# Optimization experiments

Hardware: AMD Instinct MI355X
Metric: run time of the kernel (lower is better)

Reference implementation:

```python
import jax, jax.numpy as jnp
import numpy as np

B = 256       # batch
IN_N = 64     # in_n_capsules
CS = 16       # input_size == current spatial size (child k=1,s=1,p=0)
HID = 128     # linformer hidden_dim
OUT_N = 32    # out_n_capsules
D = 16        # in_d_capsules == out_d_capsules (pose dim)
MPD = 4       # matrix_pose_dim = sqrt(D)
EPS = 1e-5
SCALE = D ** (-0.5)  # pose_dim ** -0.5 used in routing dots


def setup_inputs() -> dict:
    key = jax.random.key(0)
    ks = jax.random.split(key, 6)
    current_pose = jax.random.normal(ks[0], (B, IN_N, CS, CS, D), jnp.float32)
    next_pose = jax.random.normal(ks[1], (B, OUT_N, D), jnp.float32)
    w_current = 0.02 * jax.random.normal(ks[2], (IN_N, MPD, MPD), jnp.float32)
    w_next = 0.02 * jax.random.normal(ks[3], (OUT_N, MPD, MPD), jnp.float32)
    E_proj = 0.02 * jax.random.normal(ks[4], (IN_N, CS * CS, HID), jnp.float32)
    ln_weight = jnp.ones((D,), jnp.float32)
    ln_bias = jnp.zeros((D,), jnp.float32)
    return {
        'current_pose': current_pose, 'next_pose': next_pose,
        'w_current': w_current, 'w_next': w_next, 'E_proj': E_proj,
        'ln_weight': ln_weight, 'ln_bias': ln_bias, 'num_iter': 1,
    }


def reference(current_pose, next_pose, w_current, w_next, E_proj, ln_weight, ln_bias, num_iter):
    # ---- child matrix-pose bilinear transform ----
    # [B*CS*CS, IN_N, 4, 4] @ [1, IN_N, 4, 4]
    cp = current_pose.reshape(B * CS * CS, IN_N, MPD, MPD)
    cp = jnp.matmul(cp, w_current[None])
    # ---- Linformer headwise projection over spatial positions ----
    cp = cp.reshape(B, D, IN_N, 1, CS * CS)
    k_val = jnp.matmul(cp, E_proj[None]).squeeze(3)        # [B, D, IN_N, HID]
    k_val = k_val.reshape(B, D, IN_N * HID).transpose(0, 2, 1)  # [B, new_n, D]
    # ---- parent matrix-pose transform of next_pose (query) ----
    q = next_pose.reshape(B, OUT_N, MPD, MPD)
    q = jnp.matmul(w_next[None], q).reshape(B, OUT_N, D)   # [B, OUT_N, D]
    # ---- dot-product routing: softmax over parent capsules (dim -2) ----
    dots = jax.nn.softmax(jnp.einsum('bje,bie->bji', q, k_val) * SCALE, axis=-2)
    cand = jnp.einsum('bji,bie->bje', dots, k_val)          # [B, OUT_N, D]
    # ---- parent matrix-pose transform of candidates ----
    cand = jnp.matmul(w_next[None], cand.reshape(B, OUT_N, MPD, MPD))
    cand = cand.reshape(B, 1, 1, OUT_N, D)[:, 0]            # squeeze(1) -> [B, 1, OUT_N, D]
    # ---- dropout(p=0) is identity; LayerNorm over last dim ----
    mu = jnp.mean(cand, axis=-1, keepdims=True)
    var = jnp.mean((cand - mu) ** 2, axis=-1, keepdims=True)
    return (cand - mu) / jnp.sqrt(var + EPS) * ln_weight + ln_bias
```

## Files before the change

kernel.cpp:

```cpp
#include <hip/hip_runtime.h>
#include <cstdint>

#define EPSF 1e-5f
#define SCALEF 0.25f

typedef __attribute__((ext_vector_type(8))) __fp16 f16x8;
typedef __attribute__((ext_vector_type(2))) __fp16 f16x2;
typedef __attribute__((ext_vector_type(4))) float f32x4;

union U4H8 { uint4 u; f16x8 v; unsigned short s[8]; };
union U1H2 { unsigned u; f16x2 h; };

__device__ __forceinline__ uint32_t pk2h(float a, float b){
    union { f16x2 h; uint32_t u; } c;
    c.h = __builtin_amdgcn_cvt_pkrtz(a, b);
    return c.u;
}
__device__ __forceinline__ void gload_lds16(const void* g, void* l){
    __builtin_amdgcn_global_load_lds((const __attribute__((address_space(1))) uint32_t*)g,
                                     (__attribute__((address_space(3))) uint32_t*)l, 16, 0, 0);
}


__global__ void k_init(const float* __restrict__ wc, const float* __restrict__ E,
                       const float* __restrict__ npse, const float* __restrict__ wnx,
                       unsigned short* __restrict__ Ft, float* __restrict__ q2g){
    const int blk = blockIdx.x;
    const int tid = threadIdx.x;
    if (blk < 1024){
        const int n2 = blk >> 4, x = blk & 15;
        const int h = tid;
        const int j = (n2 & 3) * 16 + x;
        float w[16];
#pragma unroll
        for (int t = 0; t < 16; ++t) w[t] = wc[j * 16 + t];
        const float* Eb = E + ((size_t)n2 * 256 + x * 16) * 128 + h;
        float e[16];
#pragma unroll
        for (int t = 0; t < 16; ++t) e[t] = Eb[(size_t)t * 128];
        float v[16];
#pragma unroll
        for (int dd = 0; dd < 16; ++dd){
            const int r = dd >> 2, k = dd & 3;
            float acc = 0.f;
#pragma unroll
            for (int c = 0; c < 4; ++c) acc += w[k * 4 + c] * e[r * 4 + c];
            v[dd] = acc;
        }
        uint32_t pk[8];
#pragma unroll
        for (int q = 0; q < 8; ++q) pk[q] = pk2h(v[q * 2], v[q * 2 + 1]);
        unsigned short* dst = Ft + (size_t)n2 * 32768 + (size_t)h * 256 + x * 16;
        ((uint4*)dst)[0] = make_uint4(pk[0], pk[1], pk[2], pk[3]);
        ((uint4*)dst)[1] = make_uint4(pk[4], pk[5], pk[6], pk[7]);
    } else {
        const int b = blk - 1024;
#pragma unroll
        for (int q = 0; q < 4; ++q){
            const int t = q * 128 + tid;
            const int o = t >> 4, d = t & 15, r = d >> 2, c = d & 3;
            float acc = 0.f;
#pragma unroll
            for (int k = 0; k < 4; ++k)
                acc += wnx[o * 16 + r * 4 + k] * npse[((size_t)b * 32 + o) * 16 + k * 4 + c];
            q2g[(size_t)b * 512 + t] = acc * SCALEF;
        }
    }
}

__global__ __launch_bounds__(256, 4) void k_gemm(const float* __restrict__ cp,
                                                 const unsigned short* __restrict__ Ft,
                                                 const float* __restrict__ q2g,
                                                 unsigned short* __restrict__ Pmid){
    __shared__ __align__(16) char smem[40960];
    unsigned short (*As)[4096] = (unsigned short (*)[4096])smem;
    unsigned short (*Fs)[4096] = (unsigned short (*)[4096])(smem + 16384);
    const int tid  = threadIdx.x;
    const int lane = tid & 63;
    const int wave = tid >> 6;
    const int wm = wave >> 1, wn2 = wave & 1;
    const int l15 = lane & 15, g = lane >> 4;
    const int mtile = blockIdx.x;
    const int n2 = blockIdx.y;
    const int n2h = n2 >> 4, y = n2 & 15;

    const float* abase[4];
    int aoff[4];
#pragma unroll
    for (int p = 0; p < 4; ++p){
        const int idx = tid + p * 256;
        const int m = idx >> 3;
        const int kq = idx & 7;
        const int b = mtile * 8 + (m >> 4);
        const int i = (m & 15) * 4 + n2h;
        abase[p] = cp + (size_t)b * 262144 + (size_t)i * 4096 + (size_t)y * 256 + kq * 4;
        aoff[p] = m * 32 + (((kq >> 1) ^ ((m >> 1) & 3)) * 8) + (kq & 1) * 4;
    }
    const unsigned short* bsrc[2];
    unsigned short* bdst[2];
#pragma unroll
    for (int p = 0; p < 2; ++p){
        const int idx = tid + p * 256;
        const int h = idx >> 2;
        const int kq4 = idx & 3;
        bsrc[p] = Ft + (size_t)n2 * 32768 + (size_t)h * 256 + ((kq4 ^ ((h >> 1) & 3)) * 8);
        bdst[p] = &Fs[0][(size_t)(p * 256 + (tid & ~63)) * 8];
    }
    int afoff[4], bfoff[4];
#pragma unroll
    for (int mf = 0; mf < 4; ++mf){
        const int row = wm * 64 + mf * 16 + l15;
        afoff[mf] = row * 32 + ((g ^ ((row >> 1) & 3)) * 8);
    }
#pragma unroll
    for (int nf = 0; nf < 4; ++nf){
        const int row = wn2 * 64 + nf * 16 + l15;
        bfoff[nf] = row * 32 + ((g ^ ((row >> 1) & 3)) * 8);
    }

    f32x4 acc[4][4];
#pragma unroll
    for (int mf = 0; mf < 4; ++mf)
#pragma unroll
        for (int nf = 0; nf < 4; ++nf) acc[mf][nf] = (f32x4){0.f, 0.f, 0.f, 0.f};

    float4 av[4];
#pragma unroll
    for (int p = 0; p < 2; ++p) gload_lds16(bsrc[p], bdst[p]);
#pragma unroll
    for (int p = 0; p < 2; ++p) gload_lds16(bsrc[p] + 32, bdst[p] + 4096);
#pragma unroll
    for (int p = 0; p < 4; ++p) av[p] = *(const float4*)(abase[p]);
#pragma unroll
    for (int p = 0; p < 4; ++p){
        uint2 w2 = make_uint2(pk2h(av[p].x, av[p].y), pk2h(av[p].z, av[p].w));
        *(uint2*)(&As[0][aoff[p]]) = w2;
    }
    __syncthreads();

#pragma unroll
    for (int kt = 0; kt < 8; ++kt){
        if (kt < 7){
#pragma unroll
            for (int p = 0; p < 4; ++p) av[p] = *(const float4*)(abase[p] + (kt + 1) * 32);
        }
        __builtin_amdgcn_sched_barrier(0);
        if (kt < 6){
#pragma unroll
            for (int p = 0; p < 2; ++p)
                gload_lds16(bsrc[p] + (kt + 2) * 32, bdst[p] + ((kt + 2) % 3) * 4096);
        }
        f16x8 af[4], bfr[4];
#pragma unroll
        for (int mf = 0; mf < 4; ++mf) af[mf] = *(const f16x8*)(&As[kt & 1][afoff[mf]]);
#pragma unroll
        for (int nf = 0; nf < 4; ++nf) bfr[nf] = *(const f16x8*)(&Fs[kt % 3][bfoff[nf]]);
#pragma unroll
        for (int nf = 0; nf < 4; ++nf)
#pragma unroll
            for (int mf = 0; mf < 4; ++mf)
                acc[mf][nf] = __builtin_amdgcn_mfma_f32_16x16x32_f16(af[mf], bfr[nf], acc[mf][nf], 0, 0, 0);
        if (kt < 7){
#pragma unroll
            for (int p = 0; p < 4; ++p){
                uint2 w2 = make_uint2(pk2h(av[p].x, av[p].y), pk2h(av[p].z, av[p].w));
                *(uint2*)(&As[(kt + 1) & 1][aoff[p]]) = w2;
            }
        }
        if (kt < 6){ asm volatile("s_waitcnt vmcnt(2) lgkmcnt(0)" ::: "memory"); }
        else       { asm volatile("s_waitcnt vmcnt(0) lgkmcnt(0)" ::: "memory"); }
        __builtin_amdgcn_s_barrier();
        __builtin_amdgcn_sched_barrier(0);
    }

    char* eb  = smem + wave * 6144;
    char* kvT = eb;
    char* wJ  = eb + 2048;
    const f32x4 zf = (f32x4){0.f, 0.f, 0.f, 0.f};
    f32x4 pvm[4][2];

#pragma unroll
    for (int mf = 0; mf < 4; ++mf){
        const int b = mtile * 8 + wm * 4 + mf;
        U4H8 aq[2];
#pragma unroll
        for (int jh = 0; jh < 2; ++jh){
            const float4 q = *(const float4*)(q2g + (size_t)b * 512
                                              + (size_t)(jh * 16 + l15) * 16 + g * 4);
            aq[jh].u = make_uint4(pk2h(q.x, q.y), pk2h(q.z, q.w), 0u, 0u);
        }
        f32x4 pv0 = zf, pv1 = zf;
#pragma unroll
        for (int nf = 0; nf < 4; ++nf){
            U4H8 B;
            B.u = make_uint4(pk2h(acc[mf][nf][0], acc[mf][nf][1]),
                             pk2h(acc[mf][nf][2], acc[mf][nf][3]), 0u, 0u);
            const int ncol2 = (nf * 16 + l15) * 2;
#pragma unroll
            for (int r = 0; r < 4; ++r){
                const int e = g * 4 + r;
                *(unsigned short*)(kvT + e * 128 + (ncol2 ^ ((e & 7) << 4))) = B.s[r];
            }
            f32x4 s0 = __builtin_amdgcn_mfma_f32_16x16x32_f16(aq[0].v, B.v, zf, 0, 0, 0);
            f32x4 s1 = __builtin_amdgcn_mfma_f32_16x16x32_f16(aq[1].v, B.v, zf, 0, 0, 0);
            float e0[4], e1[4];
#pragma unroll
            for (int r = 0; r < 4; ++r){ e0[r] = __expf(s0[r]); e1[r] = __expf(s1[r]); }
            float ts = ((e0[0] + e0[1]) + (e0[2] + e0[3]))
                     + ((e1[0] + e1[1]) + (e1[2] + e1[3]));
            ts += __shfl_xor(ts, 16);
            ts += __shfl_xor(ts, 32);
            const float dinv = 1.f / ts;
#pragma unroll
            for (int r = 0; r < 4; ++r){
                const int j0 = 4 * g + r;
                const int sw = (j0 & 7) << 4;
                *(unsigned short*)(wJ + j0 * 128 + (ncol2 ^ sw)) =
                    (unsigned short)(pk2h(e0[r] * dinv, 0.f) & 0xFFFFu);
                *(unsigned short*)(wJ + (16 + j0) * 128 + (ncol2 ^ sw)) =
                    (unsigned short)(pk2h(e1[r] * dinv, 0.f) & 0xFFFFu);
            }
        }
#pragma unroll
        for (int kb = 0; kb < 2; ++kb){
            const int cb = kb * 64 + g * 16;
            const int swl = (l15 & 7) << 4;
            U4H8 A0, A1, Bv;
            A0.u = *(const uint4*)(wJ + l15 * 128 + (cb ^ swl));
            A1.u = *(const uint4*)(wJ + (16 + l15) * 128 + (cb ^ swl));
            Bv.u = *(const uint4*)(kvT + l15 * 128 + (cb ^ swl));
            pv0 = __builtin_amdgcn_mfma_f32_16x16x32_f16(A0.v, Bv.v, pv0, 0, 0, 0);
            pv1 = __builtin_amdgcn_mfma_f32_16x16x32_f16(A1.v, Bv.v, pv1, 0, 0, 0);
        }
        pvm[mf][0] = pv0;
        pvm[mf][1] = pv1;
    }

    __syncthreads();
    float* pvbuf = (float*)(smem + wm * 8192);
    if (wn2 == 0){
#pragma unroll
        for (int mf = 0; mf < 4; ++mf)
#pragma unroll
            for (int jh = 0; jh < 2; ++jh)
#pragma unroll
                for (int r = 0; r < 4; ++r)
                    pvbuf[mf * 512 + (jh * 16 + 4 * g + r) * 16 + l15] = pvm[mf][jh][r];
    }
    __syncthreads();
    if (wn2 == 1){
#pragma unroll
        for (int mf = 0; mf < 4; ++mf){
            const int b = mtile * 8 + wm * 4 + mf;
            unsigned short* dst = Pmid + (size_t)n2 * 131072 + (size_t)b * 512;
#pragma unroll
            for (int jh = 0; jh < 2; ++jh)
#pragma unroll
                for (int r = 0; r < 4; ++r){
                    const int idx = (jh * 16 + 4 * g + r) * 16 + l15;
                    const float sum = pvbuf[mf * 512 + idx] + pvm[mf][jh][r];
                    dst[idx] = (unsigned short)(pk2h(sum, 0.f) & 0xFFFFu);
                }
        }
    }
}

__global__ __launch_bounds__(256) void k_fin(const unsigned* __restrict__ Pmid,
                                             const float* __restrict__ wn,
                                             const float* __restrict__ lnw,
                                             const float* __restrict__ lnb,
                                             float* __restrict__ out){
    __shared__ float cnd[512];
    const int b = blockIdx.x, t = threadIdx.x;
    float s0 = 0.f, s1 = 0.f;
#pragma unroll 8
    for (int n2 = 0; n2 < 64; ++n2){
        U1H2 c; c.u = Pmid[(size_t)n2 * 65536 + (size_t)b * 256 + t];
        s0 += (float)c.h[0];
        s1 += (float)c.h[1];
    }
    cnd[2 * t]     = s0;
    cnd[2 * t + 1] = s1;
    __syncthreads();
    if (t < 32){
        const int o = t;
        float m2[16];
#pragma unroll
        for (int r = 0; r < 4; ++r)
#pragma unroll
            for (int c = 0; c < 4; ++c){
                float a = 0.f;
#pragma unroll
                for (int k = 0; k < 4; ++k)
                    a += wn[o * 16 + r * 4 + k] * cnd[o * 16 + k * 4 + c];
                m2[r * 4 + c] = a;
            }
        float mu = 0.f;
#pragma unroll
        for (int e = 0; e < 16; ++e) mu += m2[e];
        mu *= (1.f / 16.f);
        float var = 0.f;
#pragma unroll
        for (int e = 0; e < 16; ++e){ const float d = m2[e] - mu; var += d * d; }
        var *= (1.f / 16.f);
        const float invs = rsqrtf(var + EPSF);
#pragma unroll
        for (int e = 0; e < 16; ++e)
            out[(size_t)b * 512 + o * 16 + e] = (m2[e] - mu) * invs * lnw[e] + lnb[e];
    }
}

extern "C" void kernel_launch(void* const* d_in, const int* in_sizes, int n_in,
                              void* d_out, int out_size, void* d_ws, size_t ws_size,
                              hipStream_t stream){
    const float* cp   = (const float*)d_in[0];
    const float* npse = (const float*)d_in[1];
    const float* wc   = (const float*)d_in[2];
    const float* wn   = (const float*)d_in[3];
    const float* E    = (const float*)d_in[4];
    const float* lnw  = (const float*)d_in[5];
    const float* lnb  = (const float*)d_in[6];
    float* out = (float*)d_out;

    char* ws = (char*)d_ws;
    unsigned short* Ft   = (unsigned short*)ws;
    float*          q2g  = (float*)(ws + 4194304);
    unsigned short* Pmid = (unsigned short*)(ws + 4718592);

    hipLaunchKernelGGL(k_init, dim3(1280), dim3(128), 0, stream, wc, E, npse, wn, Ft, q2g);
    hipLaunchKernelGGL(k_gemm, dim3(32, 64), dim3(256), 0, stream, cp, Ft, q2g, Pmid);
    hipLaunchKernelGGL(k_fin,  dim3(256), dim3(256), 0, stream, (const unsigned*)Pmid, wn, lnw, lnb, out);
}
```

Baseline: 81.60 us.

## Split GEMM block across 16 waves with smaller per-wave tiles

Raises the k_gemm block from 256 to 1024 threads, so each of 16 waves computes a 32x32 output tile instead of 64x64 and each thread loads one A vector and at most one F vector per stage. The epilogue now gives each wave a smaller padded LDS scratch region (80-byte row stride instead of XOR swizzle) and reduces partial PV results across four waves through shared memory. The aim is more latency hiding and fewer registers per thread. In exchange, 64 KB of LDS per block limits residency, block-wide barriers now synchronise 16 waves, and the final reduction does more LDS traffic.

After: 116.4 us. 1.43x slower.

```diff
diff --git a/kernel.cpp b/kernel.cpp
--- a/kernel.cpp
+++ b/kernel.cpp
@@ -68,120 +68,98 @@
     }
 }
 
-__global__ __launch_bounds__(256, 4) void k_gemm(const float* __restrict__ cp,
-                                                 const unsigned short* __restrict__ Ft,
-                                                 const float* __restrict__ q2g,
-                                                 unsigned short* __restrict__ Pmid){
-    __shared__ __align__(16) char smem[40960];
+__global__ __launch_bounds__(1024, 8) void k_gemm(const float* __restrict__ cp,
+                                                  const unsigned short* __restrict__ Ft,
+                                                  const float* __restrict__ q2g,
+                                                  unsigned short* __restrict__ Pmid){
+    __shared__ __align__(16) char smem[65536];
     unsigned short (*As)[4096] = (unsigned short (*)[4096])smem;
     unsigned short (*Fs)[4096] = (unsigned short (*)[4096])(smem + 16384);
     const int tid  = threadIdx.x;
     const int lane = tid & 63;
     const int wave = tid >> 6;
-    const int wm = wave >> 1, wn2 = wave & 1;
+    const int wm = wave >> 2, wh = wave & 3;
     const int l15 = lane & 15, g = lane >> 4;
     const int mtile = blockIdx.x;
     const int n2 = blockIdx.y;
     const int n2h = n2 >> 4, y = n2 & 15;
 
-    const float* abase[4];
-    int aoff[4];
-#pragma unroll
-    for (int p = 0; p < 4; ++p){
-        const int idx = tid + p * 256;
-        const int m = idx >> 3;
-        const int kq = idx & 7;
-        const int b = mtile * 8 + (m >> 4);
-        const int i = (m & 15) * 4 + n2h;
-        abase[p] = cp + (size_t)b * 262144 + (size_t)i * 4096 + (size_t)y * 256 + kq * 4;
-        aoff[p] = m * 32 + (((kq >> 1) ^ ((m >> 1) & 3)) * 8) + (kq & 1) * 4;
-    }
-    const unsigned short* bsrc[2];
-    unsigned short* bdst[2];
-#pragma unroll
-    for (int p = 0; p < 2; ++p){
-        const int idx = tid + p * 256;
-        const int h = idx >> 2;
-        const int kq4 = idx & 3;
-        bsrc[p] = Ft + (size_t)n2 * 32768 + (size_t)h * 256 + ((kq4 ^ ((h >> 1) & 3)) * 8);
-        bdst[p] = &Fs[0][(size_t)(p * 256 + (tid & ~63)) * 8];
-    }
-    int afoff[4], bfoff[4];
-#pragma unroll
-    for (int mf = 0; mf < 4; ++mf){
-        const int row = wm * 64 + mf * 16 + l15;
+    const int am = tid >> 3, akq = tid & 7;
+    const float* abase = cp + (size_t)(mtile * 8 + (am >> 4)) * 262144
+                            + (size_t)((am & 15) * 4 + n2h) * 4096
+                            + (size_t)y * 256 + akq * 4;
+    const int aoff = am * 32 + (((akq >> 1) ^ ((am >> 1) & 3)) * 8) + (akq & 1) * 4;
+
+    const int bh = tid >> 2, bkq4 = tid & 3;
+    const unsigned short* bsrc = Ft + (size_t)n2 * 32768 + (size_t)bh * 256
+                                    + ((bkq4 ^ ((bh >> 1) & 3)) * 8);
+    unsigned short* bdst = &Fs[0][(size_t)(tid & ~63) * 8];
+
+    int afoff[2], bfoff[2];
+#pragma unroll
+    for (int mf = 0; mf < 2; ++mf){
+        const int row = wm * 32 + mf * 16 + l15;
         afoff[mf] = row * 32 + ((g ^ ((row >> 1) & 3)) * 8);
     }
 #pragma unroll
-    for (int nf = 0; nf < 4; ++nf){
-        const int row = wn2 * 64 + nf * 16 + l15;
+    for (int nf = 0; nf < 2; ++nf){
+        const int row = wh * 32 + nf * 16 + l15;
         bfoff[nf] = row * 32 + ((g ^ ((row >> 1) & 3)) * 8);
     }
 
-    f32x4 acc[4][4];
-#pragma unroll
-    for (int mf = 0; mf < 4; ++mf)
-#pragma unroll
-        for (int nf = 0; nf < 4; ++nf) acc[mf][nf] = (f32x4){0.f, 0.f, 0.f, 0.f};
-
-    float4 av[4];
-#pragma unroll
-    for (int p = 0; p < 2; ++p) gload_lds16(bsrc[p], bdst[p]);
-#pragma unroll
-    for (int p = 0; p < 2; ++p) gload_lds16(bsrc[p] + 32, bdst[p] + 4096);
-#pragma unroll
-    for (int p = 0; p < 4; ++p) av[p] = *(const float4*)(abase[p]);
-#pragma unroll
-    for (int p = 0; p < 4; ++p){
-        uint2 w2 = make_uint2(pk2h(av[p].x, av[p].y), pk2h(av[p].z, av[p].w));
-        *(uint2*)(&As[0][aoff[p]]) = w2;
+    f32x4 acc[2][2];
+#pragma unroll
+    for (int mf = 0; mf < 2; ++mf)
+#pragma unroll
+        for (int nf = 0; nf < 2; ++nf) acc[mf][nf] = (f32x4){0.f, 0.f, 0.f, 0.f};
+
+    float4 av;
+    if (tid < 512){
+        gload_lds16(bsrc, bdst);
+        gload_lds16(bsrc + 32, bdst + 4096);
+    }
+    av = *(const float4*)abase;
+    {
+        uint2 w2 = make_uint2(pk2h(av.x, av.y), pk2h(av.z, av.w));
+        *(uint2*)(&As[0][aoff]) = w2;
     }
     __syncthreads();
 
 #pragma unroll
     for (int kt = 0; kt < 8; ++kt){
-        if (kt < 7){
-#pragma unroll
-            for (int p = 0; p < 4; ++p) av[p] = *(const float4*)(abase[p] + (kt + 1) * 32);
-        }
+        if (kt < 7) av = *(const float4*)(abase + (kt + 1) * 32);
         __builtin_amdgcn_sched_barrier(0);
-        if (kt < 6){
-#pragma unroll
-            for (int p = 0; p < 2; ++p)
-                gload_lds16(bsrc[p] + (kt + 2) * 32, bdst[p] + ((kt + 2) % 3) * 4096);
-        }
-        f16x8 af[4], bfr[4];
-#pragma unroll
-        for (int mf = 0; mf < 4; ++mf) af[mf] = *(const f16x8*)(&As[kt & 1][afoff[mf]]);
-#pragma unroll
-        for (int nf = 0; nf < 4; ++nf) bfr[nf] = *(const f16x8*)(&Fs[kt % 3][bfoff[nf]]);
-#pragma unroll
-        for (int nf = 0; nf < 4; ++nf)
-#pragma unroll
-            for (int mf = 0; mf < 4; ++mf)
+        if (kt < 6 && tid < 512)
+            gload_lds16(bsrc + (kt + 2) * 32, bdst + ((kt + 2) % 3) * 4096);
+        f16x8 af[2], bfr[2];
+#pragma unroll
+        for (int mf = 0; mf < 2; ++mf) af[mf] = *(const f16x8*)(&As[kt & 1][afoff[mf]]);
+#pragma unroll
+        for (int nf = 0; nf < 2; ++nf) bfr[nf] = *(const f16x8*)(&Fs[kt % 3][bfoff[nf]]);
+#pragma unroll
+        for (int nf = 0; nf < 2; ++nf)
+#pragma unroll
+            for (int mf = 0; mf < 2; ++mf)
                 acc[mf][nf] = __builtin_amdgcn_mfma_f32_16x16x32_f16(af[mf], bfr[nf], acc[mf][nf], 0, 0, 0);
         if (kt < 7){
-#pragma unroll
-            for (int p = 0; p < 4; ++p){
-                uint2 w2 = make_uint2(pk2h(av[p].x, av[p].y), pk2h(av[p].z, av[p].w));
-                *(uint2*)(&As[(kt + 1) & 1][aoff[p]]) = w2;
-            }
-        }
-        if (kt < 6){ asm volatile("s_waitcnt vmcnt(2) lgkmcnt(0)" ::: "memory"); }
+            uint2 w2 = make_uint2(pk2h(av.x, av.y), pk2h(av.z, av.w));
+            *(uint2*)(&As[(kt + 1) & 1][aoff]) = w2;
+        }
+        if (kt < 6){ asm volatile("s_waitcnt vmcnt(1) lgkmcnt(0)" ::: "memory"); }
         else       { asm volatile("s_waitcnt vmcnt(0) lgkmcnt(0)" ::: "memory"); }
         __builtin_amdgcn_s_barrier();
         __builtin_amdgcn_sched_barrier(0);
     }
 
-    char* eb  = smem + wave * 6144;
+    char* eb  = smem + wave * 3840;
     char* kvT = eb;
-    char* wJ  = eb + 2048;
+    char* wJ  = eb + 1280;
     const f32x4 zf = (f32x4){0.f, 0.f, 0.f, 0.f};
-    f32x4 pvm[4][2];
-
-#pragma unroll
-    for (int mf = 0; mf < 4; ++mf){
-        const int b = mtile * 8 + wm * 4 + mf;
+    f32x4 pvm[2][2];
+
+#pragma unroll
+    for (int mf = 0; mf < 2; ++mf){
+        const int b = mtile * 8 + wm * 2 + mf;
         U4H8 aq[2];
 #pragma unroll
         for (int jh = 0; jh < 2; ++jh){
@@ -191,7 +169,7 @@
         }
         f32x4 pv0 = zf, pv1 = zf;
 #pragma unroll
-        for (int nf = 0; nf < 4; ++nf){
+        for (int nf = 0; nf < 2; ++nf){
             U4H8 B;
             B.u = make_uint4(pk2h(acc[mf][nf][0], acc[mf][nf][1]),
                              pk2h(acc[mf][nf][2], acc[mf][nf][3]), 0u, 0u);
@@ -199,7 +177,7 @@
 #pragma unroll
             for (int r = 0; r < 4; ++r){
                 const int e = g * 4 + r;
-                *(unsigned short*)(kvT + e * 128 + (ncol2 ^ ((e & 7) << 4))) = B.s[r];
+                *(unsigned short*)(kvT + e * 80 + ncol2) = B.s[r];
             }
             f32x4 s0 = __builtin_amdgcn_mfma_f32_16x16x32_f16(aq[0].v, B.v, zf, 0, 0, 0);
             f32x4 s1 = __builtin_amdgcn_mfma_f32_16x16x32_f16(aq[1].v, B.v, zf, 0, 0, 0);
@@ -214,21 +192,17 @@
 #pragma unroll
             for (int r = 0; r < 4; ++r){
                 const int j0 = 4 * g + r;
-                const int sw = (j0 & 7) << 4;
-                *(unsigned short*)(wJ + j0 * 128 + (ncol2 ^ sw)) =
+                *(unsigned short*)(wJ + j0 * 80 + ncol2) =
                     (unsigned short)(pk2h(e0[r] * dinv, 0.f) & 0xFFFFu);
-                *(unsigned short*)(wJ + (16 + j0) * 128 + (ncol2 ^ sw)) =
+                *(unsigned short*)(wJ + (16 + j0) * 80 + ncol2) =
                     (unsigned short)(pk2h(e1[r] * dinv, 0.f) & 0xFFFFu);
             }
         }
-#pragma unroll
-        for (int kb = 0; kb < 2; ++kb){
-            const int cb = kb * 64 + g * 16;
-            const int swl = (l15 & 7) << 4;
+        {
             U4H8 A0, A1, Bv;
-            A0.u = *(const uint4*)(wJ + l15 * 128 + (cb ^ swl));
-            A1.u = *(const uint4*)(wJ + (16 + l15) * 128 + (cb ^ swl));
-            Bv.u = *(const uint4*)(kvT + l15 * 128 + (cb ^ swl));
+            A0.u = *(const uint4*)(wJ + l15 * 80 + g * 16);
+            A1.u = *(const uint4*)(wJ + (16 + l15) * 80 + g * 16);
+            Bv.u = *(const uint4*)(kvT + l15 * 80 + g * 16);
             pv0 = __builtin_amdgcn_mfma_f32_16x16x32_f16(A0.v, Bv.v, pv0, 0, 0, 0);
             pv1 = __builtin_amdgcn_mfma_f32_16x16x32_f16(A1.v, Bv.v, pv1, 0, 0, 0);
         }
@@ -237,29 +211,30 @@
     }
 
     __syncthreads();
-    float* pvbuf = (float*)(smem + wm * 8192);
-    if (wn2 == 0){
-#pragma unroll
-        for (int mf = 0; mf < 4; ++mf)
-#pragma unroll
-            for (int jh = 0; jh < 2; ++jh)
-#pragma unroll
-                for (int r = 0; r < 4; ++r)
-                    pvbuf[mf * 512 + (jh * 16 + 4 * g + r) * 16 + l15] = pvm[mf][jh][r];
-    }
+    float* pvbuf = (float*)smem;
+#pragma unroll
+    for (int mf = 0; mf < 2; ++mf)
+#pragma unroll
+        for (int jh = 0; jh < 2; ++jh)
+#pragma unroll
+            for (int r = 0; r < 4; ++r)
+                pvbuf[(wave * 2 + mf) * 512 + (jh * 16 + 4 * g + r) * 16 + l15] = pvm[mf][jh][r];
     __syncthreads();
-    if (wn2 == 1){
-#pragma unroll
-        for (int mf = 0; mf < 4; ++mf){
-            const int b = mtile * 8 + wm * 4 + mf;
+    if (wh == 0){
+#pragma unroll
+        for (int mf = 0; mf < 2; ++mf){
+            const int b = mtile * 8 + wm * 2 + mf;
             unsigned short* dst = Pmid + (size_t)n2 * 131072 + (size_t)b * 512;
 #pragma unroll
             for (int jh = 0; jh < 2; ++jh)
 #pragma unroll
                 for (int r = 0; r < 4; ++r){
                     const int idx = (jh * 16 + 4 * g + r) * 16 + l15;
-                    const float sum = pvbuf[mf * 512 + idx] + pvm[mf][jh][r];
-                    dst[idx] = (unsigned short)(pk2h(sum, 0.f) & 0xFFFFu);
+                    float s = 0.f;
+#pragma unroll
+                    for (int w2 = 0; w2 < 4; ++w2)
+                        s += pvbuf[(((wm * 4 + w2) * 2) + mf) * 512 + idx];
+                    dst[idx] = (unsigned short)(pk2h(s, 0.f) & 0xFFFFu);
                 }
         }
     }
@@ -328,6 +303,6 @@
     unsigned short* Pmid = (unsigned short*)(ws + 4718592);
 
     hipLaunchKernelGGL(k_init, dim3(1280), dim3(128), 0, stream, wc, E, npse, wn, Ft, q2g);
-    hipLaunchKernelGGL(k_gemm, dim3(32, 64), dim3(256), 0, stream, cp, Ft, q2g, Pmid);
+    hipLaunchKernelGGL(k_gemm, dim3(32, 64), dim3(1024), 0, stream, cp, Ft, q2g, Pmid);
     hipLaunchKernelGGL(k_fin,  dim3(256), dim3(256), 0, stream, (const unsigned*)Pmid, wn, lnw, lnb, out);
 }
```

## Stream fp32 A tiles directly into LDS via async loads, convert at fragment read

Applied to the files above, without the earlier changes.

The A operand (fp32 current_pose) no longer goes through registers with fp16 conversion and an LDS store. It is now fetched with global_load_lds into a triple-buffered, XOR-swizzled fp32 LDS region, and converted to fp16 when the MFMA fragments are read. The B buffers drop from triple to double buffering, and the vmcnt waits and barriers are rearranged to match. LDS grows from 40 KB to 64 KB and the launch bound drops to 2 blocks per CU. This trades occupancy and larger LDS reads for asynchronous global loads that skip the register round-trip.

Result: slower. 93.89 us (+15.1%).

```diff
diff --git a/kernel.cpp b/kernel.cpp
--- a/kernel.cpp
+++ b/kernel.cpp
@@ -68,13 +68,13 @@
     }
 }
 
-__global__ __launch_bounds__(256, 4) void k_gemm(const float* __restrict__ cp,
+__global__ __launch_bounds__(256, 2) void k_gemm(const float* __restrict__ cp,
                                                  const unsigned short* __restrict__ Ft,
                                                  const float* __restrict__ q2g,
                                                  unsigned short* __restrict__ Pmid){
-    __shared__ __align__(16) char smem[40960];
-    unsigned short (*As)[4096] = (unsigned short (*)[4096])smem;
-    unsigned short (*Fs)[4096] = (unsigned short (*)[4096])(smem + 16384);
+    __shared__ __align__(16) char smem[65536];
+    char* AsB = smem;
+    char* FsB = smem + 49152;
     const int tid  = threadIdx.x;
     const int lane = tid & 63;
     const int wave = tid >> 6;
@@ -84,38 +84,40 @@
     const int n2 = blockIdx.y;
     const int n2h = n2 >> 4, y = n2 & 15;
 
-    const float* abase[4];
-    int aoff[4];
+    const float* asrc[4];
+    int adst[4];
 #pragma unroll
     for (int p = 0; p < 4; ++p){
-        const int idx = tid + p * 256;
-        const int m = idx >> 3;
-        const int kq = idx & 7;
+        const int s = p * 256 + tid;
+        const int m = s >> 3;
+        const int c16l = (s & 7) ^ (m & 7);
         const int b = mtile * 8 + (m >> 4);
         const int i = (m & 15) * 4 + n2h;
-        abase[p] = cp + (size_t)b * 262144 + (size_t)i * 4096 + (size_t)y * 256 + kq * 4;
-        aoff[p] = m * 32 + (((kq >> 1) ^ ((m >> 1) & 3)) * 8) + (kq & 1) * 4;
+        asrc[p] = cp + (size_t)b * 262144 + (size_t)i * 4096 + (size_t)y * 256 + c16l * 4;
+        adst[p] = (p * 256 + (tid & ~63)) * 16;
     }
     const unsigned short* bsrc[2];
-    unsigned short* bdst[2];
+    int bdst[2];
 #pragma unroll
     for (int p = 0; p < 2; ++p){
         const int idx = tid + p * 256;
         const int h = idx >> 2;
         const int kq4 = idx & 3;
         bsrc[p] = Ft + (size_t)n2 * 32768 + (size_t)h * 256 + ((kq4 ^ ((h >> 1) & 3)) * 8);
-        bdst[p] = &Fs[0][(size_t)(p * 256 + (tid & ~63)) * 8];
-    }
-    int afoff[4], bfoff[4];
+        bdst[p] = (p * 256 + (tid & ~63)) * 16;
+    }
+    int offA[4][2], bfoff[4];
 #pragma unroll
     for (int mf = 0; mf < 4; ++mf){
         const int row = wm * 64 + mf * 16 + l15;
-        afoff[mf] = row * 32 + ((g ^ ((row >> 1) & 3)) * 8);
+        const int x = row & 7;
+        offA[mf][0] = row * 128 + ((2 * g)     ^ x) * 16;
+        offA[mf][1] = row * 128 + ((2 * g + 1) ^ x) * 16;
     }
 #pragma unroll
     for (int nf = 0; nf < 4; ++nf){
         const int row = wn2 * 64 + nf * 16 + l15;
-        bfoff[nf] = row * 32 + ((g ^ ((row >> 1) & 3)) * 8);
+        bfoff[nf] = (row * 32 + ((g ^ ((row >> 1) & 3)) * 8)) * 2;
     }
 
     f32x4 acc[4][4];
@@ -124,54 +126,60 @@
 #pragma unroll
         for (int nf = 0; nf < 4; ++nf) acc[mf][nf] = (f32x4){0.f, 0.f, 0.f, 0.f};
 
-    float4 av[4];
-#pragma unroll
-    for (int p = 0; p < 2; ++p) gload_lds16(bsrc[p], bdst[p]);
-#pragma unroll
-    for (int p = 0; p < 2; ++p) gload_lds16(bsrc[p] + 32, bdst[p] + 4096);
-#pragma unroll
-    for (int p = 0; p < 4; ++p) av[p] = *(const float4*)(abase[p]);
-#pragma unroll
-    for (int p = 0; p < 4; ++p){
-        uint2 w2 = make_uint2(pk2h(av[p].x, av[p].y), pk2h(av[p].z, av[p].w));
-        *(uint2*)(&As[0][aoff[p]]) = w2;
-    }
-    __syncthreads();
+#pragma unroll
+    for (int p = 0; p < 4; ++p) gload_lds16(asrc[p], AsB + adst[p]);
+#pragma unroll
+    for (int p = 0; p < 2; ++p) gload_lds16(bsrc[p], FsB + bdst[p]);
+#pragma unroll
+    for (int p = 0; p < 4; ++p) gload_lds16(asrc[p] + 32, AsB + 16384 + adst[p]);
+    asm volatile("s_waitcnt vmcnt(4) lgkmcnt(0)" ::: "memory");
+    __builtin_amdgcn_s_barrier();
+    __builtin_amdgcn_sched_barrier(0);
 
 #pragma unroll
     for (int kt = 0; kt < 8; ++kt){
         if (kt < 7){
 #pragma unroll
-            for (int p = 0; p < 4; ++p) av[p] = *(const float4*)(abase[p] + (kt + 1) * 32);
-        }
-        __builtin_amdgcn_sched_barrier(0);
+            for (int p = 0; p < 2; ++p)
+                gload_lds16(bsrc[p] + (kt + 1) * 32, FsB + ((kt + 1) & 1) * 8192 + bdst[p]);
+        }
         if (kt < 6){
 #pragma unroll
-            for (int p = 0; p < 2; ++p)
-                gload_lds16(bsrc[p] + (kt + 2) * 32, bdst[p] + ((kt + 2) % 3) * 4096);
-        }
-        f16x8 af[4], bfr[4];
-#pragma unroll
-        for (int mf = 0; mf < 4; ++mf) af[mf] = *(const f16x8*)(&As[kt & 1][afoff[mf]]);
-#pragma unroll
-        for (int nf = 0; nf < 4; ++nf) bfr[nf] = *(const f16x8*)(&Fs[kt % 3][bfoff[nf]]);
-#pragma unroll
-        for (int nf = 0; nf < 4; ++nf)
-#pragma unroll
-            for (int mf = 0; mf < 4; ++mf)
-                acc[mf][nf] = __builtin_amdgcn_mfma_f32_16x16x32_f16(af[mf], bfr[nf], acc[mf][nf], 0, 0, 0);
-        if (kt < 7){
-#pragma unroll
-            for (int p = 0; p < 4; ++p){
-                uint2 w2 = make_uint2(pk2h(av[p].x, av[p].y), pk2h(av[p].z, av[p].w));
-                *(uint2*)(&As[(kt + 1) & 1][aoff[p]]) = w2;
+            for (int p = 0; p < 4; ++p)
+                gload_lds16(asrc[p] + (kt + 2) * 32, AsB + ((kt + 2) % 3) * 16384 + adst[p]);
+        }
+        {
+            const char* Ab = AsB + (kt % 3) * 16384;
+            const char* Bb = FsB + (kt & 1) * 8192;
+            f16x8 af[4], bfr[4];
+#pragma unroll
+            for (int mf = 0; mf < 4; ++mf){
+                const float4 lo = *(const float4*)(Ab + offA[mf][0]);
+                const float4 hi = *(const float4*)(Ab + offA[mf][1]);
+                U4H8 t;
+                t.u = make_uint4(pk2h(lo.x, lo.y), pk2h(lo.z, lo.w),
+                                 pk2h(hi.x, hi.y), pk2h(hi.z, hi.w));
+                af[mf] = t.v;
             }
-        }
-        if (kt < 6){ asm volatile("s_waitcnt vmcnt(2) lgkmcnt(0)" ::: "memory"); }
-        else       { asm volatile("s_waitcnt vmcnt(0) lgkmcnt(0)" ::: "memory"); }
-        __builtin_amdgcn_s_barrier();
-        __builtin_amdgcn_sched_barrier(0);
-    }
+#pragma unroll
+            for (int nf = 0; nf < 4; ++nf) bfr[nf] = *(const f16x8*)(Bb + bfoff[nf]);
+#pragma unroll
+            for (int nf = 0; nf < 4; ++nf)
+#pragma unroll
+                for (int mf = 0; mf < 4; ++mf)
+                    acc[mf][nf] = __builtin_amdgcn_mfma_f32_16x16x32_f16(af[mf], bfr[nf], acc[mf][nf], 0, 0, 0);
+        }
+        if (kt <= 5){
+            asm volatile("s_waitcnt vmcnt(4) lgkmcnt(0)" ::: "memory");
+            __builtin_amdgcn_s_barrier();
+            __builtin_amdgcn_sched_barrier(0);
+        } else if (kt == 6){
+            asm volatile("s_waitcnt vmcnt(0) lgkmcnt(0)" ::: "memory");
+            __builtin_amdgcn_s_barrier();
+            __builtin_amdgcn_sched_barrier(0);
+        }
+    }
+    __syncthreads();
 
     char* eb  = smem + wave * 6144;
     char* kvT = eb;
```
